# Kernel tuning notes

Hardware: AMD Instinct MI355X
Metric: run time of the kernel (lower is better)

The kernel has to match this reference:

```python
import jax, jax.numpy as jnp
import numpy as np

B, S, D, H = 4, 1024, 1024, 16
HD = D // H  # head_dim = 64


def setup_inputs() -> dict:
    key = jax.random.key(0)
    ks = jax.random.split(key, 9)
    scale = jnp.float32(1.0 / np.sqrt(D))
    w = lambda k: jax.random.normal(k, (D, D), jnp.float32) * scale
    return {
        "x": jax.random.normal(ks[0], (B, S, D), jnp.float32),
        "Wq_r": w(ks[1]), "Wq_i": w(ks[2]),
        "Wk_r": w(ks[3]), "Wk_i": w(ks[4]),
        "Wv_r": w(ks[5]), "Wv_i": w(ks[6]),
        "Wo_r": w(ks[7]), "Wo_i": w(ks[8]),
        "mask": jnp.ones((B, S, S), dtype=bool),
    }


def reference(x, Wq_r, Wq_i, Wk_r, Wk_i, Wv_r, Wv_i, Wo_r, Wo_i, mask):
    # Optical encoding: magnitude * exp(i * angle(x + i*roll(x,1,-1)))
    mag = jnp.abs(x)
    phase = jnp.arctan2(jnp.roll(x, 1, axis=-1), x)  # angle(x + i*rolled)
    opt = (mag * jnp.cos(phase)) + 1j * (mag * jnp.sin(phase))  # complex64 [B,S,D]

    Wq = Wq_r + 1j * Wq_i
    Wk = Wk_r + 1j * Wk_i
    Wv = Wv_r + 1j * Wv_i
    Wo = Wo_r + 1j * Wo_i

    def heads(t):  # [B,S,D] -> [B,H,S,HD]
        return jnp.transpose(t.reshape(B, S, H, HD), (0, 2, 1, 3))

    Q = heads(opt @ Wq)
    K = heads(opt @ Wk)
    V = heads(opt @ Wv)

    # Photonic correlation: abs of complex dot Q . conj(K)
    corr = jnp.einsum('bhqd,bhkd->bhqk', Q, jnp.conj(K))
    scores = jnp.abs(corr) / jnp.sqrt(jnp.float32(HD))
    scores = jnp.where(mask[:, None, :, :], scores, -jnp.inf)
    attn = jax.nn.softmax(scores, axis=-1)  # real weights [B,H,S,S]

    out = jnp.einsum('bhqk,bhkd->bhqd', attn.astype(V.dtype), V)  # complex
    out = jnp.transpose(out, (0, 2, 1, 3)).reshape(B, S, D)
    return jnp.real(out @ Wo)
```

## Files before the change

### kernel.cpp

```cpp
#include <hip/hip_runtime.h>
#include <hip/hip_bf16.h>


#define BB 4
#define SS 1024
#define DD 1024
#define HH 16
#define HD 64

typedef _Float16 f16x8 __attribute__((ext_vector_type(8)));
typedef _Float16 f16x4 __attribute__((ext_vector_type(4)));
typedef float    f32x4 __attribute__((ext_vector_type(4)));
typedef int      i32x2 __attribute__((ext_vector_type(2)));
typedef unsigned int u32x4 __attribute__((ext_vector_type(4)));

#define LOG2E 1.44269504f

__global__ __launch_bounds__(256) void k_encode_h(const float* __restrict__ x,
                                                  _Float16* __restrict__ ore,
                                                  _Float16* __restrict__ oim) {
    const int g   = blockIdx.x * 256 + threadIdx.x;
    const int row = g >> 8;
    const int d0  = (g & 255) * 4;
    const float* xr = x + (size_t)row * DD;
    const float4 xc = *(const float4*)(xr + d0);
    const float xp0 = xr[(d0 + DD - 1) & (DD - 1)];
    const float cv[4] = {xc.x, xc.y, xc.z, xc.w};
    const float pv[4] = {xp0, xc.x, xc.y, xc.z};
    f16x4 hr, hi;
    #pragma unroll
    for (int j = 0; j < 4; ++j) {
        const float r2 = cv[j]*cv[j] + pv[j]*pv[j];
        float re = 0.f, im = 0.f;
        if (r2 > 1e-30f) {
            const float inv = rsqrtf(r2);
            const float mag = fabsf(cv[j]);
            re = mag * cv[j] * inv;
            im = mag * pv[j] * inv;
        }
        hr[j] = (_Float16)re; hi[j] = (_Float16)im;
    }
    *(f16x4*)(ore + (size_t)row*DD + d0) = hr;
    *(f16x4*)(oim + (size_t)row*DD + d0) = hi;
}

__global__ __launch_bounds__(256) void k_transw8(
    const float* w0, const float* w1, const float* w2, const float* w3,
    const float* w4, const float* w5, const float* w6, const float* w7,
    _Float16* wt)
{
    __shared__ _Float16 tile[64][68];
    const float* W;
    switch (blockIdx.z) {
        case 0: W = w0; break; case 1: W = w1; break;
        case 2: W = w2; break; case 3: W = w3; break;
        case 4: W = w4; break; case 5: W = w5; break;
        case 6: W = w6; break; default: W = w7; break;
    }
    _Float16* Wt = wt + (size_t)blockIdx.z * (1u << 20);
    const int t = threadIdx.x;
    const int r = t >> 4, c4 = (t & 15) * 4;
    const int gx = blockIdx.x * 64, gy = blockIdx.y * 64;
    #pragma unroll
    for (int rr = 0; rr < 4; ++rr) {
        const float4 v = *(const float4*)(W + (size_t)(gy + r + rr*16)*DD + gx + c4);
        tile[r + rr*16][c4+0] = (_Float16)v.x;
        tile[r + rr*16][c4+1] = (_Float16)v.y;
        tile[r + rr*16][c4+2] = (_Float16)v.z;
        tile[r + rr*16][c4+3] = (_Float16)v.w;
    }
    __syncthreads();
    #pragma unroll
    for (int rr = 0; rr < 4; ++rr) {
        const int n = r + rr*16;
        f16x4 o;
        o[0] = tile[c4+0][n]; o[1] = tile[c4+1][n];
        o[2] = tile[c4+2][n]; o[3] = tile[c4+3][n];
        *(f16x4*)(Wt + (size_t)(gx + n)*DD + gy + c4) = o;
    }
}

template<int MODE>
__global__ __launch_bounds__(256, 2) void k_cgemm_h(
    const _Float16* __restrict__ Ar, const _Float16* __restrict__ Ai,
    const _Float16* __restrict__ Btr, const _Float16* __restrict__ Bti,
    _Float16* __restrict__ Cr, _Float16* __restrict__ Ci, float* __restrict__ Cf)
{
    __shared__ _Float16 lds[2][4][4096];

    const int t = threadIdx.x, w = t >> 6, l = t & 63;
    const int lr = l & 15, lg = l >> 4;

    int wg = blockIdx.x;
    wg = (wg & 7) * 32 + (wg >> 3);
    const int m0 = (wg >> 3) * 128;
    const int n0 = (wg & 7) * 128;
    const int wr = w >> 1, wc = w & 1;

    const _Float16* gbase = (w == 0) ? Ar : (w == 1) ? Ai : (w == 2) ? Btr : Bti;
    const int rowbase = (w < 2) ? m0 : n0;
    const _Float16* gp = gbase + (size_t)(rowbase + (l >> 2)) * 1024 + (l & 3) * 8;

    #define GSTAGE(K0_, BUF_)                                                         \
        {                                                                             \
            _Float16* lb = &lds[BUF_][w][0];                                          \
            _Pragma("unroll")                                                         \
            for (int i = 0; i < 8; ++i)                                               \
                __builtin_amdgcn_global_load_lds(                                     \
                    (const __attribute__((address_space(1))) void*)                   \
                        (gp + (size_t)i*16*1024 + (K0_)),                             \
                    (__attribute__((address_space(3))) void*)(lb + i*512), 16, 0, 0); \
        }

    f32x4 accR[4][4] = {};
    f32x4 accI[4][4] = {};

    GSTAGE(0, 0);
    int cur = 0;

    for (int kt = 0; kt < 32; ++kt) {
        if (kt < 31) {
            GSTAGE((kt + 1) * 32, cur ^ 1);
            asm volatile("s_waitcnt vmcnt(8)" ::: "memory");
        } else {
            asm volatile("s_waitcnt vmcnt(0)" ::: "memory");
        }
        __builtin_amdgcn_s_barrier();
        __builtin_amdgcn_sched_barrier(0);

        const _Float16* lA = &lds[cur][0][0] + (wr*64 + lr)*32 + lg*8;
        const _Float16* lB = &lds[cur][2][0] + (wc*64 + lr)*32 + lg*8;

        f16x8 ar[4], ai[4], br[4], bi[4], nai[4];
        #pragma unroll
        for (int i = 0; i < 4; ++i) {
            ar[i] = *(const f16x8*)(lA + i*512);
            ai[i] = *(const f16x8*)(lA + 4096 + i*512);
            br[i] = *(const f16x8*)(lB + i*512);
            bi[i] = *(const f16x8*)(lB + 4096 + i*512);
            union { f16x8 h; u32x4 u; } nx;
            nx.h = ai[i]; nx.u ^= 0x80008000u; nai[i] = nx.h;
        }
        __builtin_amdgcn_s_setprio(1);
        #pragma unroll
        for (int i = 0; i < 4; ++i) {
            #pragma unroll
            for (int j = 0; j < 4; ++j) {
                accR[i][j] = __builtin_amdgcn_mfma_f32_16x16x32_f16(ar[i],  br[j], accR[i][j], 0, 0, 0);
                accR[i][j] = __builtin_amdgcn_mfma_f32_16x16x32_f16(nai[i], bi[j], accR[i][j], 0, 0, 0);
                if (MODE == 0) {
                    accI[i][j] = __builtin_amdgcn_mfma_f32_16x16x32_f16(ar[i], bi[j], accI[i][j], 0, 0, 0);
                    accI[i][j] = __builtin_amdgcn_mfma_f32_16x16x32_f16(ai[i], br[j], accI[i][j], 0, 0, 0);
                }
            }
        }
        __builtin_amdgcn_s_setprio(0);
        __builtin_amdgcn_sched_barrier(0);
        __builtin_amdgcn_s_barrier();
        cur ^= 1;
    }

    #pragma unroll
    for (int i = 0; i < 4; ++i) {
        #pragma unroll
        for (int j = 0; j < 4; ++j) {
            const int m = m0 + wr*64 + i*16 + lg*4;
            const int n = n0 + wc*64 + j*16 + lr;
            #pragma unroll
            for (int r = 0; r < 4; ++r) {
                if (MODE == 0) {
                    Cr[(size_t)(m + r)*1024 + n] = (_Float16)accR[i][j][r];
                    Ci[(size_t)(m + r)*1024 + n] = (_Float16)accI[i][j][r];
                } else {
                    Cf[(size_t)(m + r)*1024 + n] = accR[i][j][r];
                }
            }
        }
    }
}

#define QB 128

__global__ __launch_bounds__(256) void k_attn4(
    const _Float16* Qre, const _Float16* Qim,
    const _Float16* __restrict__ Kre, const _Float16* __restrict__ Kim,
    const _Float16* __restrict__ Vre, const _Float16* __restrict__ Vim,
    _Float16* Ore, _Float16* Oim)
{
    __shared__ __align__(16) _Float16 lds[2][4][4096];

    const int t = threadIdx.x, w = t >> 6, l = t & 63;
    const int lr = l & 15, lg = l >> 4;
    const int bh = blockIdx.x;
    const int h = bh & (HH - 1), b = bh >> 4;
    const int qw = blockIdx.y * QB + w * 32;

    const size_t kvbase = ((size_t)(b * SS)) * DD + h * HD;

    f16x8 qr[2][2], qi[2][2], nqr[2][2];
    #pragma unroll
    for (int qs = 0; qs < 2; ++qs) {
        const size_t qoff = ((size_t)(b*SS + qw + qs*16 + lr)) * DD + h*HD + lg*8;
        #pragma unroll
        for (int ks = 0; ks < 2; ++ks) {
            qr[qs][ks] = *(const f16x8*)(Qre + qoff + 32*ks);
            qi[qs][ks] = *(const f16x8*)(Qim + qoff + 32*ks);
            union { f16x8 h; u32x4 u; } nx;
            nx.h = qr[qs][ks]; nx.u ^= 0x80008000u; nqr[qs][ks] = nx.h;
        }
    }

    const _Float16* gplane = (w == 0) ? Kre : (w == 1) ? Kim : (w == 2) ? Vre : Vim;
    const _Float16* gsrc;
    if (w < 2)
        gsrc = gplane + kvbase + (size_t)(l >> 3) * DD + ((l & 7) ^ (l >> 3)) * 8;
    else
        gsrc = gplane + kvbase + (size_t)(l >> 1) * DD + (l & 1) * 8;

    f32x4 o_re[2][4] = {}, o_im[2][4] = {};
    const float C8 = 0.18033688f;
    float m_s[2]  = {32.f, 32.f};
    float m2_s[2] = {1024.f, 1024.f};
    float mC_s[2] = {-32.f * C8, -32.f * C8};
    float l_l[2]  = {0.f, 0.f};

    #define STAGE(KT_, BUF_)                                                          \
        {                                                                             \
            _Float16* lb = &lds[BUF_][w][0];                                          \
            if (w < 2) {                                                              \
                _Pragma("unroll")                                                     \
                for (int i = 0; i < 8; ++i)                                           \
                    __builtin_amdgcn_global_load_lds(                                 \
                        (const __attribute__((address_space(1))) void*)               \
                            (gsrc + (size_t)((KT_)*64 + 8*i) * DD),                   \
                        (__attribute__((address_space(3))) void*)(lb + i*512),        \
                        16, 0, 0);                                                    \
            } else {                                                                  \
                _Pragma("unroll")                                                     \
                for (int i = 0; i < 8; ++i)                                           \
                    __builtin_amdgcn_global_load_lds(                                 \
                        (const __attribute__((address_space(1))) void*)               \
                            (gsrc + (size_t)((KT_)*64 + (i&1)*32) * DD + (i>>1)*16),  \
                        (__attribute__((address_space(3))) void*)(lb + i*512),        \
                        16, 0, 0);                                                    \
            }                                                                         \
        }

    STAGE(0, 0);
    int cur = 0;

    for (int kt = 0; kt < SS/64; ++kt) {
        if (kt < SS/64 - 1) {
            STAGE(kt + 1, cur ^ 1);
            asm volatile("s_waitcnt vmcnt(8)" ::: "memory");
        } else {
            asm volatile("s_waitcnt vmcnt(0)" ::: "memory");
        }
        __builtin_amdgcn_s_barrier();
        __builtin_amdgcn_sched_barrier(0);

        const _Float16* Kr_s = &lds[cur][0][0];
        const _Float16* Ki_s = &lds[cur][1][0];

        f32x4 dre[2][4] = {}, dim_[2][4] = {};
        #pragma unroll
        for (int st = 0; st < 4; ++st) {
            const int row = st*16 + lr;
            #pragma unroll
            for (int ks = 0; ks < 2; ++ks) {
                const int c = ((4*ks + lg) ^ (lr & 7)) * 8;
                const f16x8 kr = *(const f16x8*)(Kr_s + row*64 + c);
                const f16x8 ki = *(const f16x8*)(Ki_s + row*64 + c);
                #pragma unroll
                for (int qs = 0; qs < 2; ++qs) {
                    dre[qs][st]  = __builtin_amdgcn_mfma_f32_16x16x32_f16(kr, qr[qs][ks],  dre[qs][st],  0, 0, 0);
                    dre[qs][st]  = __builtin_amdgcn_mfma_f32_16x16x32_f16(ki, qi[qs][ks],  dre[qs][st],  0, 0, 0);
                    dim_[qs][st] = __builtin_amdgcn_mfma_f32_16x16x32_f16(kr, qi[qs][ks],  dim_[qs][st], 0, 0, 0);
                    dim_[qs][st] = __builtin_amdgcn_mfma_f32_16x16x32_f16(ki, nqr[qs][ks], dim_[qs][st], 0, 0, 0);
                }
            }
        }

        f16x4 pa[2][4];
        #pragma unroll
        for (int qs = 0; qs < 2; ++qs) {
            float d2[4][4];
            float t2 = 0.f;
            #pragma unroll
            for (int st = 0; st < 4; ++st)
                #pragma unroll
                for (int r = 0; r < 4; ++r) {
                    d2[st][r] = fmaf(dre[qs][st][r], dre[qs][st][r],
                                     dim_[qs][st][r] * dim_[qs][st][r]);
                    t2 = fmaxf(t2, d2[st][r]);
                }
            if (!__all(t2 <= m2_s[qs])) {
                float tm;
                asm("v_sqrt_f32 %0, %1" : "=v"(tm) : "v"(t2));
                tm = fmaxf(tm, __shfl_xor(tm, 16));
                tm = fmaxf(tm, __shfl_xor(tm, 32));
                const float mn = fmaxf(m_s[qs], tm);
                const float ce = (m_s[qs] - mn) * C8;
                float cq;
                asm("v_exp_f32 %0, %1" : "=v"(cq) : "v"(ce));
                l_l[qs] *= cq;
                f32x4 cT;
                #pragma unroll
                for (int r = 0; r < 4; ++r) cT[r] = __shfl(cq, lg*4 + r);
                #pragma unroll
                for (int d = 0; d < 4; ++d) { o_re[qs][d] *= cT; o_im[qs][d] *= cT; }
                m_s[qs]  = mn;
                m2_s[qs] = mn * mn;
                mC_s[qs] = -mn * C8;
            }
            float ls = 0.f;
            #pragma unroll
            for (int st = 0; st < 4; ++st)
                #pragma unroll
                for (int r = 0; r < 4; ++r) {
                    float u, p;
                    asm("v_sqrt_f32 %0, %1" : "=v"(u) : "v"(d2[st][r]));
                    const float e = fmaf(u, C8, mC_s[qs]);
                    asm("v_exp_f32 %0, %1" : "=v"(p) : "v"(e));
                    pa[qs][st][r] = (_Float16)p;
                    ls += p;
                }
            l_l[qs] += ls;
        }

        const unsigned vrb = (unsigned)(uintptr_t)&lds[cur][2][0] + 8u*l;
        const unsigned vib = (unsigned)(uintptr_t)&lds[cur][3][0] + 8u*l;
        i32x2 fr[2][4], fi[2][4];
        #pragma unroll
        for (int st = 0; st < 4; ++st) {
            const unsigned ar2 = vrb + st*512u;
            const unsigned ai2 = vib + st*512u;
            asm volatile("ds_read_b64_tr_b16 %0, %1" : "=v"(fr[0][st]) : "v"(ar2) : "memory");
            asm volatile("ds_read_b64_tr_b16 %0, %1" : "=v"(fi[0][st]) : "v"(ai2) : "memory");
        }
        #pragma unroll
        for (int d = 0; d < 4; ++d) {
            const int cb = d & 1, nb = cb ^ 1;
            if (d < 3) {
                #pragma unroll
                for (int st = 0; st < 4; ++st) {
                    const unsigned ar2 = vrb + (d+1)*2048u + st*512u;
                    const unsigned ai2 = vib + (d+1)*2048u + st*512u;
                    asm volatile("ds_read_b64_tr_b16 %0, %1" : "=v"(fr[nb][st]) : "v"(ar2) : "memory");
                    asm volatile("ds_read_b64_tr_b16 %0, %1" : "=v"(fi[nb][st]) : "v"(ai2) : "memory");
                }
                asm volatile("s_waitcnt lgkmcnt(8)" ::: "memory");
            } else {
                asm volatile("s_waitcnt lgkmcnt(0)" ::: "memory");
            }
            __builtin_amdgcn_sched_barrier(0);
            __builtin_amdgcn_s_setprio(1);
            #pragma unroll
            for (int st = 0; st < 4; ++st) {
                union { i32x2 i; f16x4 h; } cr_, ci_;
                cr_.i = fr[cb][st]; ci_.i = fi[cb][st];
                #pragma unroll
                for (int qs = 0; qs < 2; ++qs) {
                    o_re[qs][d] = __builtin_amdgcn_mfma_f32_16x16x16f16(pa[qs][st], cr_.h, o_re[qs][d], 0, 0, 0);
                    o_im[qs][d] = __builtin_amdgcn_mfma_f32_16x16x16f16(pa[qs][st], ci_.h, o_im[qs][d], 0, 0, 0);
                }
            }
            __builtin_amdgcn_s_setprio(0);
        }

        __builtin_amdgcn_sched_barrier(0);
        __builtin_amdgcn_s_barrier();
        cur ^= 1;
    }

    #pragma unroll
    for (int qs = 0; qs < 2; ++qs) {
        float lq = l_l[qs];
        lq += __shfl_xor(lq, 16);
        lq += __shfl_xor(lq, 32);
        const float inv = 1.f / lq;
        f32x4 iT;
        #pragma unroll
        for (int r = 0; r < 4; ++r) iT[r] = __shfl(inv, lg*4 + r);
        #pragma unroll
        for (int d = 0; d < 4; ++d)
            #pragma unroll
            for (int r = 0; r < 4; ++r) {
                const size_t row = (size_t)(b*SS + qw + qs*16 + lg*4 + r);
                Ore[row*DD + h*HD + d*16 + lr] = (_Float16)(o_re[qs][d][r] * iT[r]);
                Oim[row*DD + h*HD + d*16 + lr] = (_Float16)(o_im[qs][d][r] * iT[r]);
            }
    }
}

extern "C" void kernel_launch(void* const* d_in, const int* in_sizes, int n_in,
                              void* d_out, int out_size, void* d_ws, size_t ws_size,
                              hipStream_t stream) {
    const float* x   = (const float*)d_in[0];
    const float* Wqr = (const float*)d_in[1];
    const float* Wqi = (const float*)d_in[2];
    const float* Wkr = (const float*)d_in[3];
    const float* Wki = (const float*)d_in[4];
    const float* Wvr = (const float*)d_in[5];
    const float* Wvi = (const float*)d_in[6];
    const float* Wor = (const float*)d_in[7];
    const float* Woi = (const float*)d_in[8];

    const size_t P  = (size_t)BB * SS * DD;
    const size_t WP = 1u << 20;
    if (ws_size < (8 * P + 8 * WP) * sizeof(_Float16)) return;

    _Float16* wh   = (_Float16*)d_ws;
    _Float16* optR = wh;
    _Float16* optI = wh + P;
    _Float16* Qr = wh + 2*P; _Float16* Qi = wh + 3*P;
    _Float16* Kr = wh + 4*P; _Float16* Ki = wh + 5*P;
    _Float16* Vr = wh + 6*P; _Float16* Vi = wh + 7*P;
    _Float16* W8 = wh + 8*P;

    k_encode_h<<<(int)(P / 1024), 256, 0, stream>>>(x, optR, optI);
    k_transw8<<<dim3(16, 16, 8), 256, 0, stream>>>(Wqr, Wqi, Wkr, Wki, Wvr, Wvi, Wor, Woi, W8);

    k_cgemm_h<0><<<256, 256, 0, stream>>>(optR, optI, W8 + 0*WP, W8 + 1*WP, Qr, Qi, nullptr);
    k_cgemm_h<0><<<256, 256, 0, stream>>>(optR, optI, W8 + 2*WP, W8 + 3*WP, Kr, Ki, nullptr);
    k_cgemm_h<0><<<256, 256, 0, stream>>>(optR, optI, W8 + 4*WP, W8 + 5*WP, Vr, Vi, nullptr);

    k_attn4<<<dim3(BB * HH, SS / QB, 1), 256, 0, stream>>>(Qr, Qi, Kr, Ki, Vr, Vi, Qr, Qi);

    k_cgemm_h<1><<<256, 256, 0, stream>>>(Qr, Qi, W8 + 6*WP, W8 + 7*WP,
                                          nullptr, nullptr, (float*)d_out);
}
```

Baseline: 259.4 us.

## Split attention across two key halves and merge partials in a combine kernel

The attention kernel now splits the key sequence into two halves along a new grid dimension, doubling the block count to 1024. Each half writes unnormalized partial outputs plus per-row sum and max, and a new combine kernel rescales and merges them. K fragments are also loaded straight from global memory into registers instead of staging through LDS, which halves LDS use and frees shared memory. The cost is extra partial-output traffic, a second kernel launch, and uncoalesced K loads from global memory.

```diff
diff --git a/kernel.cpp b/kernel.cpp
--- a/kernel.cpp
+++ b/kernel.cpp
@@ -15,6 +15,7 @@
 typedef unsigned int u32x4 __attribute__((ext_vector_type(4)));
 
 #define LOG2E 1.44269504f
+#define C8S 0.18033688f
 
 __global__ __launch_bounds__(256) void k_encode_h(const float* __restrict__ x,
                                                   _Float16* __restrict__ ore,
@@ -181,19 +182,24 @@
 
 #define QB 128
 
-__global__ __launch_bounds__(256) void k_attn4(
-    const _Float16* Qre, const _Float16* Qim,
+__global__ __launch_bounds__(256) void k_attn5(
+    const _Float16* __restrict__ Qre, const _Float16* __restrict__ Qim,
     const _Float16* __restrict__ Kre, const _Float16* __restrict__ Kim,
     const _Float16* __restrict__ Vre, const _Float16* __restrict__ Vim,
-    _Float16* Ore, _Float16* Oim)
+    _Float16* __restrict__ PO, float* __restrict__ Lb, float* __restrict__ Mb)
 {
-    __shared__ __align__(16) _Float16 lds[2][4][4096];
+    __shared__ __align__(16) _Float16 ldsV[2][2][4096];
 
     const int t = threadIdx.x, w = t >> 6, l = t & 63;
     const int lr = l & 15, lg = l >> 4;
     const int bh = blockIdx.x;
     const int h = bh & (HH - 1), b = bh >> 4;
     const int qw = blockIdx.y * QB + w * 32;
+    const int z  = blockIdx.z;
+    const int kt0 = z * 8, kt1 = kt0 + 8;
+    const size_t PLANE = (size_t)BB * SS * DD;
+    _Float16* Por = PO + (size_t)z * 2 * PLANE;
+    _Float16* Poi = Por + PLANE;
 
     const size_t kvbase = ((size_t)(b * SS)) * DD + h * HD;
 
@@ -210,73 +216,65 @@
         }
     }
 
-    const _Float16* gplane = (w == 0) ? Kre : (w == 1) ? Kim : (w == 2) ? Vre : Vim;
-    const _Float16* gsrc;
-    if (w < 2)
-        gsrc = gplane + kvbase + (size_t)(l >> 3) * DD + ((l & 7) ^ (l >> 3)) * 8;
-    else
-        gsrc = gplane + kvbase + (size_t)(l >> 1) * DD + (l & 1) * 8;
+    const _Float16* krp = Kre + kvbase + (size_t)lr * DD + lg * 8;
+    const _Float16* kip = Kim + kvbase + (size_t)lr * DD + lg * 8;
+
+    const _Float16* vsrc = ((w < 2) ? Vre : Vim) + kvbase + (size_t)(l >> 1) * DD + (l & 1) * 8;
+    const int hp = w & 1;
+
+    #define STAGEV(KT_, BUF_)                                                         \
+        {                                                                             \
+            _Float16* lb = &ldsV[BUF_][w >> 1][0];                                    \
+            _Pragma("unroll")                                                         \
+            for (int ii = 0; ii < 4; ++ii) {                                          \
+                const int ip = hp * 4 + ii;                                           \
+                __builtin_amdgcn_global_load_lds(                                     \
+                    (const __attribute__((address_space(1))) void*)                   \
+                        (vsrc + (size_t)((KT_)*64 + (ip&1)*32) * DD + (ip>>1)*16),    \
+                    (__attribute__((address_space(3))) void*)(lb + ip*512), 16, 0, 0);\
+            }                                                                         \
+        }
 
     f32x4 o_re[2][4] = {}, o_im[2][4] = {};
-    const float C8 = 0.18033688f;
     float m_s[2]  = {32.f, 32.f};
     float m2_s[2] = {1024.f, 1024.f};
-    float mC_s[2] = {-32.f * C8, -32.f * C8};
+    float mC_s[2] = {-32.f * C8S, -32.f * C8S};
     float l_l[2]  = {0.f, 0.f};
 
-    #define STAGE(KT_, BUF_)                                                          \
-        {                                                                             \
-            _Float16* lb = &lds[BUF_][w][0];                                          \
-            if (w < 2) {                                                              \
-                _Pragma("unroll")                                                     \
-                for (int i = 0; i < 8; ++i)                                           \
-                    __builtin_amdgcn_global_load_lds(                                 \
-                        (const __attribute__((address_space(1))) void*)               \
-                            (gsrc + (size_t)((KT_)*64 + 8*i) * DD),                   \
-                        (__attribute__((address_space(3))) void*)(lb + i*512),        \
-                        16, 0, 0);                                                    \
-            } else {                                                                  \
-                _Pragma("unroll")                                                     \
-                for (int i = 0; i < 8; ++i)                                           \
-                    __builtin_amdgcn_global_load_lds(                                 \
-                        (const __attribute__((address_space(1))) void*)               \
-                            (gsrc + (size_t)((KT_)*64 + (i&1)*32) * DD + (i>>1)*16),  \
-                        (__attribute__((address_space(3))) void*)(lb + i*512),        \
-                        16, 0, 0);                                                    \
-            }                                                                         \
-        }
-
-    STAGE(0, 0);
+    STAGEV(kt0, 0);
     int cur = 0;
 
-    for (int kt = 0; kt < SS/64; ++kt) {
-        if (kt < SS/64 - 1) {
-            STAGE(kt + 1, cur ^ 1);
-            asm volatile("s_waitcnt vmcnt(8)" ::: "memory");
+    for (int kt = kt0; kt < kt1; ++kt) {
+        f16x8 krf[4][2], kif[4][2];
+        #pragma unroll
+        for (int st = 0; st < 4; ++st) {
+            #pragma unroll
+            for (int ks = 0; ks < 2; ++ks) {
+                const size_t o = (size_t)(kt*64 + st*16) * DD + ks*32;
+                krf[st][ks] = *(const f16x8*)(krp + o);
+                kif[st][ks] = *(const f16x8*)(kip + o);
+            }
+        }
+        if (kt < kt1 - 1) {
+            STAGEV(kt + 1, cur ^ 1);
+            asm volatile("s_waitcnt vmcnt(20)" ::: "memory");
         } else {
-            asm volatile("s_waitcnt vmcnt(0)" ::: "memory");
+            asm volatile("s_waitcnt vmcnt(16)" ::: "memory");
         }
         __builtin_amdgcn_s_barrier();
         __builtin_amdgcn_sched_barrier(0);
 
-        const _Float16* Kr_s = &lds[cur][0][0];
-        const _Float16* Ki_s = &lds[cur][1][0];
-
         f32x4 dre[2][4] = {}, dim_[2][4] = {};
         #pragma unroll
         for (int st = 0; st < 4; ++st) {
-            const int row = st*16 + lr;
             #pragma unroll
             for (int ks = 0; ks < 2; ++ks) {
-                const int c = ((4*ks + lg) ^ (lr & 7)) * 8;
-                const f16x8 kr = *(const f16x8*)(Kr_s + row*64 + c);
-                const f16x8 ki = *(const f16x8*)(Ki_s + row*64 + c);
                 #pragma unroll
                 for (int qs = 0; qs < 2; ++qs) {
-                    dre[qs][st]  = __builtin_amdgcn_mfma_f32_16x16x32_f16(kr, qr[qs][ks],  dre[qs][st],  0, 0, 0);
-                    dre[qs][st]  = __builtin_amdgcn_mfma_f32_16x16x32_f16(ki, qi[qs][ks],  dre[qs][st],  0, 0, 0);
-                    dim_[qs][st] = __builtin_amdgcn_mfma_f32_16x16x32_f16(kr, qi[qs][ks],  dim_[qs][st], 0, 0, 0);
-                    dim_[qs][st] = __builtin_amdgcn_mfma_f32_16x16x32_f16(ki, nqr[qs][ks], dim_[qs][st], 0, 0, 0);
+                    dre[qs][st]  = __builtin_amdgcn_mfma_f32_16x16x32_f16(krf[st][ks], qr[qs][ks],  dre[qs][st],  0, 0, 0);
+                    dre[qs][st]  = __builtin_amdgcn_mfma_f32_16x16x32_f16(kif[st][ks], qi[qs][ks],  dre[qs][st],  0, 0, 0);
+                    dim_[qs][st] = __builtin_amdgcn_mfma_f32_16x16x32_f16(krf[st][ks], qi[qs][ks],  dim_[qs][st], 0, 0, 0);
+                    dim_[qs][st] = __builtin_amdgcn_mfma_f32_16x16x32_f16(kif[st][ks], nqr[qs][ks], dim_[qs][st], 0, 0, 0);
                 }
             }
         }
@@ -300,7 +298,7 @@
                 tm = fmaxf(tm, __shfl_xor(tm, 16));
                 tm = fmaxf(tm, __shfl_xor(tm, 32));
                 const float mn = fmaxf(m_s[qs], tm);
-                const float ce = (m_s[qs] - mn) * C8;
+                const float ce = (m_s[qs] - mn) * C8S;
                 float cq;
                 asm("v_exp_f32 %0, %1" : "=v"(cq) : "v"(ce));
                 l_l[qs] *= cq;
@@ -311,7 +309,7 @@
                 for (int d = 0; d < 4; ++d) { o_re[qs][d] *= cT; o_im[qs][d] *= cT; }
                 m_s[qs]  = mn;
                 m2_s[qs] = mn * mn;
-                mC_s[qs] = -mn * C8;
+                mC_s[qs] = -mn * C8S;
             }
             float ls = 0.f;
             #pragma unroll
@@ -320,7 +318,7 @@
                 for (int r = 0; r < 4; ++r) {
                     float u, p;
                     asm("v_sqrt_f32 %0, %1" : "=v"(u) : "v"(d2[st][r]));
-                    const float e = fmaf(u, C8, mC_s[qs]);
+                    const float e = fmaf(u, C8S, mC_s[qs]);
                     asm("v_exp_f32 %0, %1" : "=v"(p) : "v"(e));
                     pa[qs][st][r] = (_Float16)p;
                     ls += p;
@@ -328,15 +326,13 @@
             l_l[qs] += ls;
         }
 
-        const unsigned vrb = (unsigned)(uintptr_t)&lds[cur][2][0] + 8u*l;
-        const unsigned vib = (unsigned)(uintptr_t)&lds[cur][3][0] + 8u*l;
+        const unsigned vrb = (unsigned)(uintptr_t)&ldsV[cur][0][0] + 8u*l;
+        const unsigned vib = (unsigned)(uintptr_t)&ldsV[cur][1][0] + 8u*l;
         i32x2 fr[2][4], fi[2][4];
         #pragma unroll
         for (int st = 0; st < 4; ++st) {
-            const unsigned ar2 = vrb + st*512u;
-            const unsigned ai2 = vib + st*512u;
-            asm volatile("ds_read_b64_tr_b16 %0, %1" : "=v"(fr[0][st]) : "v"(ar2) : "memory");
-            asm volatile("ds_read_b64_tr_b16 %0, %1" : "=v"(fi[0][st]) : "v"(ai2) : "memory");
+            asm volatile("ds_read_b64_tr_b16 %0, %1" : "=v"(fr[0][st]) : "v"(vrb + st*512u) : "memory");
+            asm volatile("ds_read_b64_tr_b16 %0, %1" : "=v"(fi[0][st]) : "v"(vib + st*512u) : "memory");
         }
         #pragma unroll
         for (int d = 0; d < 4; ++d) {
@@ -344,10 +340,8 @@
             if (d < 3) {
                 #pragma unroll
                 for (int st = 0; st < 4; ++st) {
-                    const unsigned ar2 = vrb + (d+1)*2048u + st*512u;
-                    const unsigned ai2 = vib + (d+1)*2048u + st*512u;
-                    asm volatile("ds_read_b64_tr_b16 %0, %1" : "=v"(fr[nb][st]) : "v"(ar2) : "memory");
-                    asm volatile("ds_read_b64_tr_b16 %0, %1" : "=v"(fi[nb][st]) : "v"(ai2) : "memory");
+                    asm volatile("ds_read_b64_tr_b16 %0, %1" : "=v"(fr[nb][st]) : "v"(vrb + (d+1)*2048u + st*512u) : "memory");
+                    asm volatile("ds_read_b64_tr_b16 %0, %1" : "=v"(fi[nb][st]) : "v"(vib + (d+1)*2048u + st*512u) : "memory");
                 }
                 asm volatile("s_waitcnt lgkmcnt(8)" ::: "memory");
             } else {
@@ -378,19 +372,52 @@
         float lq = l_l[qs];
         lq += __shfl_xor(lq, 16);
         lq += __shfl_xor(lq, 32);
-        const float inv = 1.f / lq;
-        f32x4 iT;
-        #pragma unroll
-        for (int r = 0; r < 4; ++r) iT[r] = __shfl(inv, lg*4 + r);
+        if (l < 16) {
+            const int q = qw + qs*16 + lr;
+            Lb[z * 65536 + (bh << 10) + q] = lq;
+            Mb[z * 65536 + (bh << 10) + q] = m_s[qs];
+        }
         #pragma unroll
         for (int d = 0; d < 4; ++d)
             #pragma unroll
             for (int r = 0; r < 4; ++r) {
                 const size_t row = (size_t)(b*SS + qw + qs*16 + lg*4 + r);
-                Ore[row*DD + h*HD + d*16 + lr] = (_Float16)(o_re[qs][d][r] * iT[r]);
-                Oim[row*DD + h*HD + d*16 + lr] = (_Float16)(o_im[qs][d][r] * iT[r]);
-            }
-    }
+                Por[row*DD + h*HD + d*16 + lr] = (_Float16)o_re[qs][d][r];
+                Poi[row*DD + h*HD + d*16 + lr] = (_Float16)o_im[qs][d][r];
+            }
+    }
+}
+
+__global__ __launch_bounds__(256) void k_combine(
+    const _Float16* __restrict__ P0r, const _Float16* __restrict__ P0i,
+    const _Float16* __restrict__ P1r, const _Float16* __restrict__ P1i,
+    const float* __restrict__ Lb, const float* __restrict__ Mb,
+    _Float16* __restrict__ Or, _Float16* __restrict__ Oi)
+{
+    const int u = blockIdx.x * 256 + threadIdx.x;
+    const int row = u >> 7;
+    const int c8  = u & 127;
+    const int hh  = c8 >> 3;
+    const int q = row & 1023, b = row >> 10;
+    const int li = ((b * 16 + hh) << 10) + q;
+    const float l0 = Lb[li], l1 = Lb[65536 + li];
+    const float m0 = Mb[li], m1 = Mb[65536 + li];
+    const float mm = fmaxf(m0, m1);
+    const float f0 = exp2f((m0 - mm) * C8S);
+    const float f1 = exp2f((m1 - mm) * C8S);
+    const float inv = 1.f / fmaf(l0, f0, l1 * f1);
+    const float s0 = f0 * inv, s1 = f1 * inv;
+    const size_t off = (size_t)row * DD + c8 * 8;
+    const f16x8 a0 = *(const f16x8*)(P0r + off), a1 = *(const f16x8*)(P1r + off);
+    const f16x8 b0 = *(const f16x8*)(P0i + off), b1 = *(const f16x8*)(P1i + off);
+    f16x8 xr, xi;
+    #pragma unroll
+    for (int j = 0; j < 8; ++j) {
+        xr[j] = (_Float16)fmaf((float)a0[j], s0, (float)a1[j] * s1);
+        xi[j] = (_Float16)fmaf((float)b0[j], s0, (float)b1[j] * s1);
+    }
+    *(f16x8*)(Or + off) = xr;
+    *(f16x8*)(Oi + off) = xi;
 }
 
 extern "C" void kernel_launch(void* const* d_in, const int* in_sizes, int n_in,
@@ -408,7 +435,8 @@
 
     const size_t P  = (size_t)BB * SS * DD;
     const size_t WP = 1u << 20;
-    if (ws_size < (8 * P + 8 * WP) * sizeof(_Float16)) return;
+    const size_t need = (12 * P + 8 * WP) * sizeof(_Float16) + 4ull * 4 * 65536;
+    if (ws_size < need) return;
 
     _Float16* wh   = (_Float16*)d_ws;
     _Float16* optR = wh;
@@ -417,6 +445,10 @@
     _Float16* Kr = wh + 4*P; _Float16* Ki = wh + 5*P;
     _Float16* Vr = wh + 6*P; _Float16* Vi = wh + 7*P;
     _Float16* W8 = wh + 8*P;
+    _Float16* PO = wh + 8*P + 8*WP;
+    float*    LM = (float*)(wh + 12*P + 8*WP);
+    float*    Lb = LM;
+    float*    Mb = LM + 131072;
 
     k_encode_h<<<(int)(P / 1024), 256, 0, stream>>>(x, optR, optI);
     k_transw8<<<dim3(16, 16, 8), 256, 0, stream>>>(Wqr, Wqi, Wkr, Wki, Wvr, Wvi, Wor, Woi, W8);
@@ -425,7 +457,11 @@
     k_cgemm_h<0><<<256, 256, 0, stream>>>(optR, optI, W8 + 2*WP, W8 + 3*WP, Kr, Ki, nullptr);
     k_cgemm_h<0><<<256, 256, 0, stream>>>(optR, optI, W8 + 4*WP, W8 + 5*WP, Vr, Vi, nullptr);
 
-    k_attn4<<<dim3(BB * HH, SS / QB, 1), 256, 0, stream>>>(Qr, Qi, Kr, Ki, Vr, Vi, Qr, Qi);
+    k_attn5<<<dim3(BB * HH, SS / QB, 2), 256, 0, stream>>>(
+        Qr, Qi, Kr, Ki, Vr, Vi, PO, Lb, Mb);
+
+    k_combine<<<2048, 256, 0, stream>>>(PO, PO + P, PO + 2*P, PO + 3*P,
+                                        Lb, Mb, Qr, Qi);
 
     k_cgemm_h<1><<<256, 256, 0, stream>>>(Qr, Qi, W8 + 6*WP, W8 + 7*WP,
                                           nullptr, nullptr, (float*)d_out);
```

New measurement: 323.7 us. 1.25x slower.
